# Optimization experiments

Measured on AMD Instinct MI355X. Metric: run time of the kernel, lower is better.

Reference implementation:

```python
import jax, jax.numpy as jnp
import numpy as np

N_GRAPHS = 256

def setup_inputs() -> dict:
    key = jax.random.key(0)
    ks = jax.random.split(key, 8)
    N, E, C, H, L, O = 50000, 800000, 128, 128, 3, 1
    s = 1.0 / np.sqrt(H)
    x = jax.random.normal(ks[0], (N, C), jnp.float32)
    edge_index = jax.random.randint(ks[1], (2, E), 0, N)
    batch = jnp.sort(jax.random.randint(ks[2], (N,), 0, N_GRAPHS))
    W1 = jax.random.normal(ks[3], (L, C, H), jnp.float32) * s
    b1 = jnp.zeros((L, H), jnp.float32)
    W2 = jax.random.normal(ks[4], (L, H, H), jnp.float32) * s
    b2 = jnp.zeros((L, H), jnp.float32)
    eps = jnp.zeros((L,), jnp.float32)
    Wh = jax.random.normal(ks[5], (H, O), jnp.float32) * s
    bh = jnp.zeros((O,), jnp.float32)
    return dict(x=x, edge_index=edge_index, batch=batch, W1=W1, b1=b1,
                W2=W2, b2=b2, eps=eps, Wh=Wh, bh=bh)

def reference(x, edge_index, batch, W1, b1, W2, b2, eps, Wh, bh):
    # GIN (PyG BasicGNN, norm=None): per layer h = MLP((1+eps)*h + sum_{j->i} h_j),
    # MLP = Linear -> ReLU -> Linear; ReLU (+dropout, identity at eval) between layers.
    src, dst = edge_index[0], edge_index[1]
    N = x.shape[0]
    L = W1.shape[0]
    h = x
    for l in range(L):
        agg = jax.ops.segment_sum(h[src], dst, num_segments=N)   # [N, H] scatter-add
        z = (1.0 + eps[l]) * h + agg
        z = jnp.maximum(z @ W1[l] + b1[l], 0.0) @ W2[l] + b2[l]
        h = jnp.maximum(z, 0.0) if l < L - 1 else z
    # global_mean_pool over graph ids
    sums = jax.ops.segment_sum(h, batch, num_segments=N_GRAPHS)
    cnt = jax.ops.segment_sum(jnp.ones((N,), h.dtype), batch, num_segments=N_GRAPHS)
    pooled = sums / jnp.maximum(cnt, 1.0)[:, None]               # [G, H]
    return pooled @ Wh + bh                                      # [G, out_channels]
```

## Files before the change

kernel.cpp:

```cpp
#include <hip/hip_runtime.h>
#include <cstdint>

#define H 128
#define NGRAPH 256
#define ROWSTRIDE 68
#define NPB 256
#define CSR_CAP 6144

typedef __attribute__((ext_vector_type(8))) short short8;
typedef __attribute__((ext_vector_type(4))) float floatx4;

typedef unsigned short u16;
typedef unsigned int u32;

__device__ __forceinline__ u16 f2b(float f) {
    union { float f; u32 u; } v; v.f = f;
    u32 r = v.u + 0x7fffu + ((v.u >> 16) & 1u);
    return (u16)(r >> 16);
}
__device__ __forceinline__ float lo_f(u32 v) {
    union { u32 u; float f; } w; w.u = v << 16; return w.f;
}
__device__ __forceinline__ float hi_f(u32 v) {
    union { u32 u; float f; } w; w.u = v & 0xffff0000u; return w.f;
}

__global__ void convert_kernel(const float* __restrict__ in, u16* __restrict__ out, int n4) {
    int i = blockIdx.x * blockDim.x + threadIdx.x;
    if (i < n4) {
        float4 v = *(const float4*)(in + (size_t)i * 4);
        u16 o[4] = { f2b(v.x), f2b(v.y), f2b(v.z), f2b(v.w) };
        *(uint2*)(out + (size_t)i * 4) = *(uint2*)o;
    }
}

__global__ void pack_w_kernel(const float* __restrict__ W1, const float* __restrict__ W2,
                              u16* __restrict__ packed, int total) {
    int idx = blockIdx.x * blockDim.x + threadIdx.x;
    if (idx >= total) return;
    int mat = idx >> 14;
    int pos = idx & 16383;
    int j    = pos & 7;
    int lane = (pos >> 3) & 63;
    int nt   = (pos >> 9) & 7;
    int kc   = pos >> 12;
    int k = kc * 32 + (lane >> 4) * 8 + j;
    int n = nt * 16 + (lane & 15);
    const float* src = (mat < 3) ? (W1 + (size_t)mat * H * H) : (W2 + (size_t)(mat - 3) * H * H);
    packed[idx] = f2b(src[(size_t)k * H + n]);
}

__global__ __launch_bounds__(256) void bucket_hist(const int* __restrict__ dstv,
                                                   int* __restrict__ bcnt, int E, int NB) {
    __shared__ int sh[256];
    int t = threadIdx.x;
    sh[t] = 0;
    __syncthreads();
    for (int e = blockIdx.x * 256 + t; e < E; e += gridDim.x * 256)
        atomicAdd(&sh[dstv[e] >> 8], 1);
    __syncthreads();
    if (t < NB && sh[t] > 0) atomicAdd(&bcnt[t], sh[t]);
}

__global__ void bucket_scan(const int* __restrict__ bcnt, int* __restrict__ boffs,
                            int* __restrict__ bcursor, int NB) {
    if (threadIdx.x == 0 && blockIdx.x == 0) {
        int run = 0;
        for (int i = 0; i < NB; ++i) { boffs[i] = run; bcursor[i] = run; run += bcnt[i]; }
        boffs[NB] = run;
    }
}

#define SCHUNK 4096
__global__ __launch_bounds__(256) void scatter_kernel(const int* __restrict__ src,
                                                      const int* __restrict__ dstv,
                                                      int* __restrict__ bcursor,
                                                      u32* __restrict__ stage, int E, int NB) {
    __shared__ int lcnt[256];
    __shared__ int lbase[256];
    int t = threadIdx.x;
    lcnt[t] = 0;
    __syncthreads();
    int base = blockIdx.x * SCHUNK;
    u32 pk[16];
    int bk[16];
#pragma unroll
    for (int i = 0; i < 16; ++i) {
        int idx = base + t + i * 256;
        bk[i] = -1;
        if (idx < E) {
            int s = src[idx];
            int d = dstv[idx];
            int b = d >> 8;
            pk[i] = (u32)s | ((u32)(d & 255) << 24);
            bk[i] = b;
            atomicAdd(&lcnt[b], 1);
        }
    }
    __syncthreads();
    if (t < NB && lcnt[t] > 0) lbase[t] = atomicAdd(&bcursor[t], lcnt[t]);
    __syncthreads();
    lcnt[t] = 0;
    __syncthreads();
#pragma unroll
    for (int i = 0; i < 16; ++i) {
        if (bk[i] >= 0) {
            int r = atomicAdd(&lcnt[bk[i]], 1);
            stage[(size_t)lbase[bk[i]] + r] = pk[i];
        }
    }
}

__global__ __launch_bounds__(256) void build_csr(const u32* __restrict__ stage,
                                                 const int* __restrict__ boffs,
                                                 int* __restrict__ offs, int* __restrict__ cols,
                                                 int N, int NB, int E) {
    __shared__ int cnt[256];
    __shared__ int cur[256];
    __shared__ int sA[256];
    __shared__ int sB[256];
    __shared__ int colstage[CSR_CAP];
    int b = blockIdx.x;
    int t = threadIdx.x;
    int lo = boffs[b], hi = boffs[b + 1];
    int sz = hi - lo;
    int nlo = b * NPB;
    cnt[t] = 0;
    __syncthreads();
    for (int i = t; i < sz; i += 256) atomicAdd(&cnt[stage[(size_t)lo + i] >> 24], 1);
    __syncthreads();
    sA[t] = cnt[t];
    __syncthreads();
    int* a = sA; int* bb = sB;
    for (int off = 1; off < 256; off <<= 1) {
        bb[t] = (t >= off) ? (a[t] + a[t - off]) : a[t];
        __syncthreads();
        int* tmp = a; a = bb; bb = tmp;
    }
    int excl = a[t] - cnt[t];
    if (nlo + t < N) offs[nlo + t] = lo + excl;
    if (b == 0 && t == 0) offs[N] = E;
    cur[t] = excl;
    __syncthreads();
    if (sz <= CSR_CAP) {
        for (int i = t; i < sz; i += 256) {
            u32 pk = stage[(size_t)lo + i];
            int r = atomicAdd(&cur[pk >> 24], 1);
            colstage[r] = (int)(pk & 0xFFFFFFu);
        }
        __syncthreads();
        for (int i = t; i < sz; i += 256) cols[(size_t)lo + i] = colstage[i];
    } else {
        for (int i = t; i < sz; i += 256) {
            u32 pk = stage[(size_t)lo + i];
            int r = atomicAdd(&cur[pk >> 24], 1);
            cols[(size_t)lo + r] = (int)(pk & 0xFFFFFFu);
        }
    }
}

__global__ __launch_bounds__(256) void fused_layer(const u16* __restrict__ h,
                                                   u16* __restrict__ hout,
                                                   const int* __restrict__ offs,
                                                   const int* __restrict__ cols,
                                                   const u16* __restrict__ Wp1,
                                                   const u16* __restrict__ Wp2,
                                                   const float* __restrict__ bias1,
                                                   const float* __restrict__ bias2,
                                                   const float* __restrict__ eps, int layer,
                                                   int relu2, int N) {
    __shared__ u32 ldsA[16 * ROWSTRIDE];
    __shared__ u32 ldsB[16 * ROWSTRIDE];

    const int tid = threadIdx.x;
    const int wave = tid >> 6;
    const int lane = tid & 63;
    const int m = lane & 15;
    const int quad = lane >> 4;
    const int nt0 = wave * 2, nt1 = wave * 2 + 1;
    const int row0 = blockIdx.x * 16;

    const float scale = 1.0f + eps[layer];
    const u32* __restrict__ hp = (const u32*)h;

    {
        const int nid = wave * 4 + quad;
        const int node = row0 + nid;
        float a[8];
#pragma unroll
        for (int i = 0; i < 8; ++i) a[i] = 0.f;
        if (node < N) {
#pragma unroll
            for (int i = 0; i < 4; ++i) {
                u32 v = hp[(size_t)node * 64 + m + 16 * i];
                a[2 * i]     = scale * lo_f(v);
                a[2 * i + 1] = scale * hi_f(v);
            }
            int beg = offs[node], end = offs[node + 1];
            int j = beg;
            for (; j + 2 <= end; j += 2) {
                int c0 = cols[j], c1 = cols[j + 1];
                u32 v0[4], v1[4];
#pragma unroll
                for (int i = 0; i < 4; ++i) v0[i] = hp[(size_t)c0 * 64 + m + 16 * i];
#pragma unroll
                for (int i = 0; i < 4; ++i) v1[i] = hp[(size_t)c1 * 64 + m + 16 * i];
#pragma unroll
                for (int i = 0; i < 4; ++i) {
                    a[2 * i]     += lo_f(v0[i]) + lo_f(v1[i]);
                    a[2 * i + 1] += hi_f(v0[i]) + hi_f(v1[i]);
                }
            }
            if (j < end) {
                int c0 = cols[j];
#pragma unroll
                for (int i = 0; i < 4; ++i) {
                    u32 v = hp[(size_t)c0 * 64 + m + 16 * i];
                    a[2 * i]     += lo_f(v);
                    a[2 * i + 1] += hi_f(v);
                }
            }
        }
#pragma unroll
        for (int i = 0; i < 4; ++i) {
            u16 p[2] = { f2b(a[2 * i]), f2b(a[2 * i + 1]) };
            ldsA[nid * ROWSTRIDE + m + 16 * i] = *(u32*)p;
        }
    }

    short8 B1f0[4], B1f1[4], B2f0[4], B2f1[4];
#pragma unroll
    for (int kc = 0; kc < 4; ++kc) {
        B1f0[kc] = *(const short8*)(Wp1 + ((size_t)(kc * 8 + nt0) * 64 + lane) * 8);
        B1f1[kc] = *(const short8*)(Wp1 + ((size_t)(kc * 8 + nt1) * 64 + lane) * 8);
        B2f0[kc] = *(const short8*)(Wp2 + ((size_t)(kc * 8 + nt0) * 64 + lane) * 8);
        B2f1[kc] = *(const short8*)(Wp2 + ((size_t)(kc * 8 + nt1) * 64 + lane) * 8);
    }
    const int cg0 = nt0 * 16 + m, cg1 = nt1 * 16 + m;
    const float b1v0 = bias1[cg0], b1v1 = bias1[cg1];
    const float b2v0 = bias2[cg0], b2v1 = bias2[cg1];
    __syncthreads();

    {
        short8 a0 = *(const short8*)(&ldsA[m * ROWSTRIDE + 0 * 16 + quad * 4]);
        short8 a1 = *(const short8*)(&ldsA[m * ROWSTRIDE + 1 * 16 + quad * 4]);
        short8 a2 = *(const short8*)(&ldsA[m * ROWSTRIDE + 2 * 16 + quad * 4]);
        short8 a3 = *(const short8*)(&ldsA[m * ROWSTRIDE + 3 * 16 + quad * 4]);
        floatx4 acc0 = {0.f, 0.f, 0.f, 0.f};
        floatx4 acc1 = {0.f, 0.f, 0.f, 0.f};
        acc0 = __builtin_amdgcn_mfma_f32_16x16x32_bf16(a0, B1f0[0], acc0, 0, 0, 0);
        acc1 = __builtin_amdgcn_mfma_f32_16x16x32_bf16(a0, B1f1[0], acc1, 0, 0, 0);
        acc0 = __builtin_amdgcn_mfma_f32_16x16x32_bf16(a1, B1f0[1], acc0, 0, 0, 0);
        acc1 = __builtin_amdgcn_mfma_f32_16x16x32_bf16(a1, B1f1[1], acc1, 0, 0, 0);
        acc0 = __builtin_amdgcn_mfma_f32_16x16x32_bf16(a2, B1f0[2], acc0, 0, 0, 0);
        acc1 = __builtin_amdgcn_mfma_f32_16x16x32_bf16(a2, B1f1[2], acc1, 0, 0, 0);
        acc0 = __builtin_amdgcn_mfma_f32_16x16x32_bf16(a3, B1f0[3], acc0, 0, 0, 0);
        acc1 = __builtin_amdgcn_mfma_f32_16x16x32_bf16(a3, B1f1[3], acc1, 0, 0, 0);
        u16* lb = (u16*)ldsB;
#pragma unroll
        for (int i = 0; i < 4; ++i) {
            int rr = quad * 4 + i;
            lb[rr * (ROWSTRIDE * 2) + cg0] = f2b(fmaxf(acc0[i] + b1v0, 0.f));
            lb[rr * (ROWSTRIDE * 2) + cg1] = f2b(fmaxf(acc1[i] + b1v1, 0.f));
        }
    }
    __syncthreads();

    {
        short8 a0 = *(const short8*)(&ldsB[m * ROWSTRIDE + 0 * 16 + quad * 4]);
        short8 a1 = *(const short8*)(&ldsB[m * ROWSTRIDE + 1 * 16 + quad * 4]);
        short8 a2 = *(const short8*)(&ldsB[m * ROWSTRIDE + 2 * 16 + quad * 4]);
        short8 a3 = *(const short8*)(&ldsB[m * ROWSTRIDE + 3 * 16 + quad * 4]);
        floatx4 acc0 = {0.f, 0.f, 0.f, 0.f};
        floatx4 acc1 = {0.f, 0.f, 0.f, 0.f};
        acc0 = __builtin_amdgcn_mfma_f32_16x16x32_bf16(a0, B2f0[0], acc0, 0, 0, 0);
        acc1 = __builtin_amdgcn_mfma_f32_16x16x32_bf16(a0, B2f1[0], acc1, 0, 0, 0);
        acc0 = __builtin_amdgcn_mfma_f32_16x16x32_bf16(a1, B2f0[1], acc0, 0, 0, 0);
        acc1 = __builtin_amdgcn_mfma_f32_16x16x32_bf16(a1, B2f1[1], acc1, 0, 0, 0);
        acc0 = __builtin_amdgcn_mfma_f32_16x16x32_bf16(a2, B2f0[2], acc0, 0, 0, 0);
        acc1 = __builtin_amdgcn_mfma_f32_16x16x32_bf16(a2, B2f1[2], acc1, 0, 0, 0);
        acc0 = __builtin_amdgcn_mfma_f32_16x16x32_bf16(a3, B2f0[3], acc0, 0, 0, 0);
        acc1 = __builtin_amdgcn_mfma_f32_16x16x32_bf16(a3, B2f1[3], acc1, 0, 0, 0);
        u16* la = (u16*)ldsA;
#pragma unroll
        for (int i = 0; i < 4; ++i) {
            int rr = quad * 4 + i;
            float v0 = acc0[i] + b2v0;
            float v1 = acc1[i] + b2v1;
            if (relu2) { v0 = fmaxf(v0, 0.f); v1 = fmaxf(v1, 0.f); }
            la[rr * (ROWSTRIDE * 2) + cg0] = f2b(v0);
            la[rr * (ROWSTRIDE * 2) + cg1] = f2b(v1);
        }
    }
    __syncthreads();

    {
        int rr = tid >> 4;
        int s  = tid & 15;
        int grow = row0 + rr;
        if (grow < N) {
            uint4 v = *(uint4*)(&ldsA[rr * ROWSTRIDE + s * 4]);
            *(uint4*)(hout + (size_t)grow * H + s * 8) = v;
        }
    }
}

__global__ __launch_bounds__(256) void dot_kernel(const u16* __restrict__ h,
                                                  const float* __restrict__ Wh,
                                                  float* __restrict__ y, int N) {
    int node = blockIdx.x * 4 + (threadIdx.x >> 6);
    if (node >= N) return;
    int lane = threadIdx.x & 63;
    u32 hv = *(const u32*)(h + (size_t)node * H + lane * 2);
    float v = lo_f(hv) * Wh[lane * 2] + hi_f(hv) * Wh[lane * 2 + 1];
#pragma unroll
    for (int off = 32; off > 0; off >>= 1) v += __shfl_down(v, off);
    if (lane == 0) y[node] = v;
}

__device__ __forceinline__ int lbound(const int* __restrict__ a, int n, int v) {
    int lo = 0, hi = n;
    while (lo < hi) { int mid = (lo + hi) >> 1; if (a[mid] < v) lo = mid + 1; else hi = mid; }
    return lo;
}

__global__ void seg_out_kernel(const float* __restrict__ y, const int* __restrict__ batch,
                               const float* __restrict__ bh, float* __restrict__ out, int N) {
    __shared__ float sh[256];
    int g = blockIdx.x;
    int lo = lbound(batch, N, g);
    int hi = lbound(batch, N, g + 1);
    float s = 0.f;
    for (int i = lo + threadIdx.x; i < hi; i += 256) s += y[i];
    sh[threadIdx.x] = s;
    __syncthreads();
    for (int off = 128; off > 0; off >>= 1) {
        if (threadIdx.x < off) sh[threadIdx.x] += sh[threadIdx.x + off];
        __syncthreads();
    }
    if (threadIdx.x == 0) {
        float cnt = (float)(hi - lo);
        out[g] = sh[0] / fmaxf(cnt, 1.0f) + bh[0];
    }
}

extern "C" void kernel_launch(void* const* d_in, const int* in_sizes, int n_in,
                              void* d_out, int out_size, void* d_ws, size_t ws_size,
                              hipStream_t stream) {
    const float* x    = (const float*)d_in[0];
    const int*   eidx = (const int*)d_in[1];
    const int*   batch= (const int*)d_in[2];
    const float* W1   = (const float*)d_in[3];
    const float* b1   = (const float*)d_in[4];
    const float* W2   = (const float*)d_in[5];
    const float* b2   = (const float*)d_in[6];
    const float* eps  = (const float*)d_in[7];
    const float* Wh   = (const float*)d_in[8];
    const float* bh   = (const float*)d_in[9];

    const int N = in_sizes[0] / H;
    const int E = in_sizes[1] / 2;
    const int L = in_sizes[7];
    const int* src  = eidx;
    const int* dstv = eidx + E;
    float* out = (float*)d_out;

    const int NB = (N + NPB - 1) / NPB;

    char* w = (char*)d_ws;
    u16* B0 = (u16*)w; w += (size_t)N * H * sizeof(u16);
    u16* B1 = (u16*)w; w += (size_t)N * H * sizeof(u16);
    u16* packedW = (u16*)w; w += (size_t)6 * H * H * sizeof(u16);
    float* y    = (float*)w; w += (size_t)N * sizeof(float);
    int* offs   = (int*)w;   w += (size_t)(N + 1) * sizeof(int);
    int* bcnt   = (int*)w;   w += 256 * sizeof(int);
    int* boffs  = (int*)w;   w += 257 * sizeof(int);
    int* bcursor= (int*)w;   w += 256 * sizeof(int);
    u32* stage  = (u32*)w;   w += (size_t)E * sizeof(u32);
    int* cols   = (int*)w;   w += (size_t)E * sizeof(int);

    hipMemsetAsync(bcnt, 0, 256 * sizeof(int), stream);

    {
        int n4 = N * H / 4;
        convert_kernel<<<(n4 + 255) / 256, 256, 0, stream>>>(x, B0, n4);
    }
    {
        int total = 6 * H * H;
        pack_w_kernel<<<(total + 255) / 256, 256, 0, stream>>>(W1, W2, packedW, total);
    }
    bucket_hist<<<256, 256, 0, stream>>>(dstv, bcnt, E, NB);
    bucket_scan<<<1, 64, 0, stream>>>(bcnt, boffs, bcursor, NB);
    scatter_kernel<<<(E + SCHUNK - 1) / SCHUNK, 256, 0, stream>>>(src, dstv, bcursor, stage, E, NB);
    build_csr<<<NB, 256, 0, stream>>>(stage, boffs, offs, cols, N, NB, E);

    const int numTiles = (N + 15) / 16;
    u16* bufs[2] = { B0, B1 };
    int cur = 0;
    for (int l = 0; l < L; ++l) {
        int nxt = cur ^ 1;
        fused_layer<<<numTiles, 256, 0, stream>>>(bufs[cur], bufs[nxt], offs, cols,
                                                  packedW + (size_t)l * H * H,
                                                  packedW + (size_t)(3 + l) * H * H,
                                                  b1 + (size_t)l * H, b2 + (size_t)l * H,
                                                  eps, l, (l < L - 1) ? 1 : 0, N);
        cur = nxt;
    }

    dot_kernel<<<(N + 3) / 4, 256, 0, stream>>>(bufs[cur], Wh, y, N);
    seg_out_kernel<<<NGRAPH, 256, 0, stream>>>(y, batch, bh, out, N);
}
```

Baseline: 280.1 us.

## Fuse head dot into last GIN layer and gather rows wave-wide

```diff
diff --git a/kernel.cpp b/kernel.cpp
--- a/kernel.cpp
+++ b/kernel.cpp
@@ -17,6 +17,10 @@
     union { float f; u32 u; } v; v.f = f;
     u32 r = v.u + 0x7fffu + ((v.u >> 16) & 1u);
     return (u16)(r >> 16);
+}
+__device__ __forceinline__ float b2f(u16 b) {
+    union { u32 u; float f; } v; v.u = ((u32)b) << 16;
+    return v.f;
 }
 __device__ __forceinline__ float lo_f(u32 v) {
     union { u32 u; float f; } w; w.u = v << 16; return w.f;
@@ -168,9 +172,12 @@
                                                    const float* __restrict__ bias1,
                                                    const float* __restrict__ bias2,
                                                    const float* __restrict__ eps, int layer,
-                                                   int relu2, int N) {
+                                                   int relu2, int lastLayer,
+                                                   const float* __restrict__ Wh,
+                                                   float* __restrict__ y, int N) {
     __shared__ u32 ldsA[16 * ROWSTRIDE];
     __shared__ u32 ldsB[16 * ROWSTRIDE];
+    __shared__ float dacc[16];
 
     const int tid = threadIdx.x;
     const int wave = tid >> 6;
@@ -183,49 +190,37 @@
     const float scale = 1.0f + eps[layer];
     const u32* __restrict__ hp = (const u32*)h;
 
-    {
-        const int nid = wave * 4 + quad;
-        const int node = row0 + nid;
-        float a[8];
-#pragma unroll
-        for (int i = 0; i < 8; ++i) a[i] = 0.f;
+#pragma unroll
+    for (int nn = 0; nn < 4; ++nn) {
+        const int node = row0 + wave * 4 + nn;
+        float ax = 0.f, ay = 0.f, bx = 0.f, by = 0.f;
         if (node < N) {
-#pragma unroll
-            for (int i = 0; i < 4; ++i) {
-                u32 v = hp[(size_t)node * 64 + m + 16 * i];
-                a[2 * i]     = scale * lo_f(v);
-                a[2 * i + 1] = scale * hi_f(v);
-            }
+            u32 hv = hp[(size_t)node * 64 + lane];
+            ax = scale * lo_f(hv);
+            ay = scale * hi_f(hv);
             int beg = offs[node], end = offs[node + 1];
             int j = beg;
-            for (; j + 2 <= end; j += 2) {
-                int c0 = cols[j], c1 = cols[j + 1];
-                u32 v0[4], v1[4];
-#pragma unroll
-                for (int i = 0; i < 4; ++i) v0[i] = hp[(size_t)c0 * 64 + m + 16 * i];
-#pragma unroll
-                for (int i = 0; i < 4; ++i) v1[i] = hp[(size_t)c1 * 64 + m + 16 * i];
-#pragma unroll
-                for (int i = 0; i < 4; ++i) {
-                    a[2 * i]     += lo_f(v0[i]) + lo_f(v1[i]);
-                    a[2 * i + 1] += hi_f(v0[i]) + hi_f(v1[i]);
-                }
+            for (; j + 4 <= end; j += 4) {
+                int c0 = cols[j], c1 = cols[j + 1], c2 = cols[j + 2], c3 = cols[j + 3];
+                u32 v0 = hp[(size_t)c0 * 64 + lane];
+                u32 v1 = hp[(size_t)c1 * 64 + lane];
+                u32 v2 = hp[(size_t)c2 * 64 + lane];
+                u32 v3 = hp[(size_t)c3 * 64 + lane];
+                ax += lo_f(v0) + lo_f(v2);
+                ay += hi_f(v0) + hi_f(v2);
+                bx += lo_f(v1) + lo_f(v3);
+                by += hi_f(v1) + hi_f(v3);
             }
-            if (j < end) {
-                int c0 = cols[j];
-#pragma unroll
-                for (int i = 0; i < 4; ++i) {
-                    u32 v = hp[(size_t)c0 * 64 + m + 16 * i];
-                    a[2 * i]     += lo_f(v);
-                    a[2 * i + 1] += hi_f(v);
-                }
+            for (; j < end; ++j) {
+                u32 v = hp[(size_t)cols[j] * 64 + lane];
+                ax += lo_f(v);
+                ay += hi_f(v);
             }
-        }
-#pragma unroll
-        for (int i = 0; i < 4; ++i) {
-            u16 p[2] = { f2b(a[2 * i]), f2b(a[2 * i + 1]) };
-            ldsA[nid * ROWSTRIDE + m + 16 * i] = *(u32*)p;
-        }
+            ax += bx;
+            ay += by;
+        }
+        u16 p[2] = { f2b(ax), f2b(ay) };
+        ldsA[(wave * 4 + nn) * ROWSTRIDE + lane] = *(u32*)p;
     }
 
     short8 B1f0[4], B1f1[4], B2f0[4], B2f1[4];
@@ -263,6 +258,7 @@
             lb[rr * (ROWSTRIDE * 2) + cg0] = f2b(fmaxf(acc0[i] + b1v0, 0.f));
             lb[rr * (ROWSTRIDE * 2) + cg1] = f2b(fmaxf(acc1[i] + b1v1, 0.f));
         }
+        if (tid < 16) dacc[tid] = 0.f;
     }
     __syncthreads();
 
@@ -281,41 +277,45 @@
         acc1 = __builtin_amdgcn_mfma_f32_16x16x32_bf16(a2, B2f1[2], acc1, 0, 0, 0);
         acc0 = __builtin_amdgcn_mfma_f32_16x16x32_bf16(a3, B2f0[3], acc0, 0, 0, 0);
         acc1 = __builtin_amdgcn_mfma_f32_16x16x32_bf16(a3, B2f1[3], acc1, 0, 0, 0);
-        u16* la = (u16*)ldsA;
-#pragma unroll
-        for (int i = 0; i < 4; ++i) {
-            int rr = quad * 4 + i;
-            float v0 = acc0[i] + b2v0;
-            float v1 = acc1[i] + b2v1;
-            if (relu2) { v0 = fmaxf(v0, 0.f); v1 = fmaxf(v1, 0.f); }
-            la[rr * (ROWSTRIDE * 2) + cg0] = f2b(v0);
-            la[rr * (ROWSTRIDE * 2) + cg1] = f2b(v1);
-        }
-    }
-    __syncthreads();
-
-    {
-        int rr = tid >> 4;
-        int s  = tid & 15;
-        int grow = row0 + rr;
-        if (grow < N) {
-            uint4 v = *(uint4*)(&ldsA[rr * ROWSTRIDE + s * 4]);
-            *(uint4*)(hout + (size_t)grow * H + s * 8) = v;
-        }
-    }
-}
-
-__global__ __launch_bounds__(256) void dot_kernel(const u16* __restrict__ h,
-                                                  const float* __restrict__ Wh,
-                                                  float* __restrict__ y, int N) {
-    int node = blockIdx.x * 4 + (threadIdx.x >> 6);
-    if (node >= N) return;
-    int lane = threadIdx.x & 63;
-    u32 hv = *(const u32*)(h + (size_t)node * H + lane * 2);
-    float v = lo_f(hv) * Wh[lane * 2] + hi_f(hv) * Wh[lane * 2 + 1];
-#pragma unroll
-    for (int off = 32; off > 0; off >>= 1) v += __shfl_down(v, off);
-    if (lane == 0) y[node] = v;
+
+        if (!lastLayer) {
+            u16* la = (u16*)ldsA;
+#pragma unroll
+            for (int i = 0; i < 4; ++i) {
+                int rr = quad * 4 + i;
+                float v0 = acc0[i] + b2v0;
+                float v1 = acc1[i] + b2v1;
+                if (relu2) { v0 = fmaxf(v0, 0.f); v1 = fmaxf(v1, 0.f); }
+                la[rr * (ROWSTRIDE * 2) + cg0] = f2b(v0);
+                la[rr * (ROWSTRIDE * 2) + cg1] = f2b(v1);
+            }
+            __syncthreads();
+            int rr = tid >> 4;
+            int s  = tid & 15;
+            int grow = row0 + rr;
+            if (grow < N) {
+                uint4 v = *(uint4*)(&ldsA[rr * ROWSTRIDE + s * 4]);
+                *(uint4*)(hout + (size_t)grow * H + s * 8) = v;
+            }
+        } else {
+            const float wh0 = Wh[cg0], wh1 = Wh[cg1];
+            float part[4];
+#pragma unroll
+            for (int i = 0; i < 4; ++i)
+                part[i] = b2f(f2b(acc0[i] + b2v0)) * wh0 +
+                          b2f(f2b(acc1[i] + b2v1)) * wh1;
+#pragma unroll
+            for (int off = 1; off < 16; off <<= 1)
+#pragma unroll
+                for (int i = 0; i < 4; ++i) part[i] += __shfl_xor(part[i], off, 64);
+            if (m == 0) {
+#pragma unroll
+                for (int i = 0; i < 4; ++i) atomicAdd(&dacc[quad * 4 + i], part[i]);
+            }
+            __syncthreads();
+            if (tid < 16 && row0 + tid < N) y[row0 + tid] = dacc[tid];
+        }
+    }
 }
 
 __device__ __forceinline__ int lbound(const int* __restrict__ a, int n, int v) {
@@ -399,14 +399,15 @@
     int cur = 0;
     for (int l = 0; l < L; ++l) {
         int nxt = cur ^ 1;
+        int last = (l == L - 1) ? 1 : 0;
         fused_layer<<<numTiles, 256, 0, stream>>>(bufs[cur], bufs[nxt], offs, cols,
                                                   packedW + (size_t)l * H * H,
                                                   packedW + (size_t)(3 + l) * H * H,
                                                   b1 + (size_t)l * H, b2 + (size_t)l * H,
-                                                  eps, l, (l < L - 1) ? 1 : 0, N);
+                                                  eps, l, (l < L - 1) ? 1 : 0, last,
+                                                  Wh, y, N);
         cur = nxt;
     }
 
-    dot_kernel<<<(N + 3) / 4, 256, 0, stream>>>(bufs[cur], Wh, y, N);
     seg_out_kernel<<<NGRAPH, 256, 0, stream>>>(y, batch, bh, out, N);
 }
```

After: 318.0 us. 13.6% more time.

## Fuse head dot-product into last GIN layer and unroll neighbor gather by four

Applied to the files above, without the earlier changes.

```diff
diff --git a/kernel.cpp b/kernel.cpp
--- a/kernel.cpp
+++ b/kernel.cpp
@@ -17,6 +17,10 @@
     union { float f; u32 u; } v; v.f = f;
     u32 r = v.u + 0x7fffu + ((v.u >> 16) & 1u);
     return (u16)(r >> 16);
+}
+__device__ __forceinline__ float b2f(u16 b) {
+    union { u32 u; float f; } v; v.u = ((u32)b) << 16;
+    return v.f;
 }
 __device__ __forceinline__ float lo_f(u32 v) {
     union { u32 u; float f; } w; w.u = v << 16; return w.f;
@@ -168,9 +172,12 @@
                                                    const float* __restrict__ bias1,
                                                    const float* __restrict__ bias2,
                                                    const float* __restrict__ eps, int layer,
-                                                   int relu2, int N) {
+                                                   int relu2, int lastLayer,
+                                                   const float* __restrict__ Wh,
+                                                   float* __restrict__ y, int N) {
     __shared__ u32 ldsA[16 * ROWSTRIDE];
     __shared__ u32 ldsB[16 * ROWSTRIDE];
+    __shared__ float dacc[16];
 
     const int tid = threadIdx.x;
     const int wave = tid >> 6;
@@ -198,20 +205,24 @@
             }
             int beg = offs[node], end = offs[node + 1];
             int j = beg;
-            for (; j + 2 <= end; j += 2) {
-                int c0 = cols[j], c1 = cols[j + 1];
-                u32 v0[4], v1[4];
+            for (; j + 4 <= end; j += 4) {
+                int c0 = cols[j], c1 = cols[j + 1], c2 = cols[j + 2], c3 = cols[j + 3];
+                u32 v0[4], v1[4], v2[4], v3[4];
 #pragma unroll
                 for (int i = 0; i < 4; ++i) v0[i] = hp[(size_t)c0 * 64 + m + 16 * i];
 #pragma unroll
                 for (int i = 0; i < 4; ++i) v1[i] = hp[(size_t)c1 * 64 + m + 16 * i];
 #pragma unroll
+                for (int i = 0; i < 4; ++i) v2[i] = hp[(size_t)c2 * 64 + m + 16 * i];
+#pragma unroll
+                for (int i = 0; i < 4; ++i) v3[i] = hp[(size_t)c3 * 64 + m + 16 * i];
+#pragma unroll
                 for (int i = 0; i < 4; ++i) {
-                    a[2 * i]     += lo_f(v0[i]) + lo_f(v1[i]);
-                    a[2 * i + 1] += hi_f(v0[i]) + hi_f(v1[i]);
+                    a[2 * i]     += (lo_f(v0[i]) + lo_f(v1[i])) + (lo_f(v2[i]) + lo_f(v3[i]));
+                    a[2 * i + 1] += (hi_f(v0[i]) + hi_f(v1[i])) + (hi_f(v2[i]) + hi_f(v3[i]));
                 }
             }
-            if (j < end) {
+            for (; j < end; ++j) {
                 int c0 = cols[j];
 #pragma unroll
                 for (int i = 0; i < 4; ++i) {
@@ -263,6 +274,7 @@
             lb[rr * (ROWSTRIDE * 2) + cg0] = f2b(fmaxf(acc0[i] + b1v0, 0.f));
             lb[rr * (ROWSTRIDE * 2) + cg1] = f2b(fmaxf(acc1[i] + b1v1, 0.f));
         }
+        if (tid < 16) dacc[tid] = 0.f;
     }
     __syncthreads();
 
@@ -281,41 +293,45 @@
         acc1 = __builtin_amdgcn_mfma_f32_16x16x32_bf16(a2, B2f1[2], acc1, 0, 0, 0);
         acc0 = __builtin_amdgcn_mfma_f32_16x16x32_bf16(a3, B2f0[3], acc0, 0, 0, 0);
         acc1 = __builtin_amdgcn_mfma_f32_16x16x32_bf16(a3, B2f1[3], acc1, 0, 0, 0);
-        u16* la = (u16*)ldsA;
-#pragma unroll
-        for (int i = 0; i < 4; ++i) {
-            int rr = quad * 4 + i;
-            float v0 = acc0[i] + b2v0;
-            float v1 = acc1[i] + b2v1;
-            if (relu2) { v0 = fmaxf(v0, 0.f); v1 = fmaxf(v1, 0.f); }
-            la[rr * (ROWSTRIDE * 2) + cg0] = f2b(v0);
-            la[rr * (ROWSTRIDE * 2) + cg1] = f2b(v1);
-        }
-    }
-    __syncthreads();
-
-    {
-        int rr = tid >> 4;
-        int s  = tid & 15;
-        int grow = row0 + rr;
-        if (grow < N) {
-            uint4 v = *(uint4*)(&ldsA[rr * ROWSTRIDE + s * 4]);
-            *(uint4*)(hout + (size_t)grow * H + s * 8) = v;
-        }
-    }
-}
-
-__global__ __launch_bounds__(256) void dot_kernel(const u16* __restrict__ h,
-                                                  const float* __restrict__ Wh,
-                                                  float* __restrict__ y, int N) {
-    int node = blockIdx.x * 4 + (threadIdx.x >> 6);
-    if (node >= N) return;
-    int lane = threadIdx.x & 63;
-    u32 hv = *(const u32*)(h + (size_t)node * H + lane * 2);
-    float v = lo_f(hv) * Wh[lane * 2] + hi_f(hv) * Wh[lane * 2 + 1];
-#pragma unroll
-    for (int off = 32; off > 0; off >>= 1) v += __shfl_down(v, off);
-    if (lane == 0) y[node] = v;
+
+        if (!lastLayer) {
+            u16* la = (u16*)ldsA;
+#pragma unroll
+            for (int i = 0; i < 4; ++i) {
+                int rr = quad * 4 + i;
+                float v0 = acc0[i] + b2v0;
+                float v1 = acc1[i] + b2v1;
+                if (relu2) { v0 = fmaxf(v0, 0.f); v1 = fmaxf(v1, 0.f); }
+                la[rr * (ROWSTRIDE * 2) + cg0] = f2b(v0);
+                la[rr * (ROWSTRIDE * 2) + cg1] = f2b(v1);
+            }
+            __syncthreads();
+            int rr = tid >> 4;
+            int s  = tid & 15;
+            int grow = row0 + rr;
+            if (grow < N) {
+                uint4 v = *(uint4*)(&ldsA[rr * ROWSTRIDE + s * 4]);
+                *(uint4*)(hout + (size_t)grow * H + s * 8) = v;
+            }
+        } else {
+            const float wh0 = Wh[cg0], wh1 = Wh[cg1];
+            float part[4];
+#pragma unroll
+            for (int i = 0; i < 4; ++i)
+                part[i] = b2f(f2b(acc0[i] + b2v0)) * wh0 +
+                          b2f(f2b(acc1[i] + b2v1)) * wh1;
+#pragma unroll
+            for (int off = 1; off < 16; off <<= 1)
+#pragma unroll
+                for (int i = 0; i < 4; ++i) part[i] += __shfl_xor(part[i], off, 64);
+            if (m == 0) {
+#pragma unroll
+                for (int i = 0; i < 4; ++i) atomicAdd(&dacc[quad * 4 + i], part[i]);
+            }
+            __syncthreads();
+            if (tid < 16 && row0 + tid < N) y[row0 + tid] = dacc[tid];
+        }
+    }
 }
 
 __device__ __forceinline__ int lbound(const int* __restrict__ a, int n, int v) {
@@ -399,14 +415,15 @@
     int cur = 0;
     for (int l = 0; l < L; ++l) {
         int nxt = cur ^ 1;
+        int last = (l == L - 1) ? 1 : 0;
         fused_layer<<<numTiles, 256, 0, stream>>>(bufs[cur], bufs[nxt], offs, cols,
                                                   packedW + (size_t)l * H * H,
                                                   packedW + (size_t)(3 + l) * H * H,
                                                   b1 + (size_t)l * H, b2 + (size_t)l * H,
-                                                  eps, l, (l < L - 1) ? 1 : 0, N);
+                                                  eps, l, (l < L - 1) ? 1 : 0, last,
+                                                  Wh, y, N);
         cur = nxt;
     }
 
-    dot_kernel<<<(N + 3) / 4, 256, 0, stream>>>(bufs[cur], Wh, y, N);
     seg_out_kernel<<<NGRAPH, 256, 0, stream>>>(y, batch, bh, out, N);
 }
```

Measured after the change: 258.6 us. 1.08x faster.
